# Optimization experiments

Hardware: AMD Instinct MI355X
Metric: run time of the kernel (lower is better)

Reference implementation:

```python
import jax, jax.numpy as jnp
import numpy as np

B, DIN, N = 8, 256, 2048  # batch, input_dim (orig node_num), attention nodes (orig seq_len)


def setup_inputs() -> dict:
    key = jax.random.key(0)
    k1, k2, k3, k4 = jax.random.split(key, 4)
    x = jax.random.normal(k1, (B, DIN, N), jnp.float32)
    adj = jax.random.randint(k2, (N, N), 0, 2).astype(jnp.int32)  # binary adjacency
    W = jax.random.normal(k3, (DIN, DIN), jnp.float32) * 0.05      # Linear(D, D, bias=False), stored (out, in)
    a = jax.random.normal(k4, (3 * DIN,), jnp.float32) * 0.05      # Linear(3D, 1, bias=False)
    return {"x": x, "adj": adj, "W": W, "a": a}


def reference(x, adj, W, a):
    # x: (B, D, N) -> permute to (B, N, D); attention is over the N axis
    xt = jnp.transpose(x, (0, 2, 1))
    h = xt @ W.T                                   # (B, N, D)
    sim = jnp.einsum('bid,bjd->bij', h, h)         # (B, N, N) pairwise dot products
    n = adj.shape[0]
    # neighbor mask: adj nonzero, diagonal forced off (mask[:, i] = 0 in the loop)
    m = (adj != 0) & (~jnp.eye(n, dtype=bool))
    # context: the torch loop's weighted_h is independent of its k axis, so
    # context[b, k, i, d] == C[b, i, d] = sum_j m[i,j] * sim[b,i,j] * h[b,j,d]
    C = jnp.einsum('bij,bjd->bid', jnp.where(m[None, :, :], sim, 0.0), h)  # (B, N, D)
    d = h.shape[-1]
    a1, a2, a3 = a[:d], a[d:2 * d], a[2 * d:]
    # a([h_i, h_j, C_j]) = a1.h_i + a2.h_j + a3.C_j  (concat never materialized)
    s_i = h @ a1                                   # (B, N)
    s_j = h @ a2 + C @ a3                          # (B, N)
    scores = jax.nn.leaky_relu(s_i[:, :, None] + s_j[:, None, :], negative_slope=0.2)
    scores = jnp.where(adj[None, :, :] == 0, jnp.float32(-9e15), scores)
    return jax.nn.softmax(scores, axis=-1)         # (B, N, N)
```

## Files before the change

### kernel.cpp

```cpp
#include <hip/hip_runtime.h>
#include <hip/hip_bf16.h>
#include <math.h>

#define Bq   8
#define DINq 256
#define Nq   2048

typedef __attribute__((ext_vector_type(8))) short bf16x8v;
typedef __attribute__((ext_vector_type(4))) float f32x4v;

__device__ __forceinline__ unsigned short f2bf(float f) {
  union { float f; unsigned u; } v; v.f = f;
  unsigned r = v.u + 0x7fffu + ((v.u >> 16) & 1u);
  return (unsigned short)(r >> 16);
}
__device__ __forceinline__ float bf2f(unsigned short h) {
  union { unsigned u; float f; } v; v.u = ((unsigned)h) << 16;
  return v.f;
}

__device__ __forceinline__ void gld_lds16(const void* g, void* l) {
  __builtin_amdgcn_global_load_lds(
      (const __attribute__((address_space(1))) unsigned int*)g,
      (__attribute__((address_space(3))) unsigned int*)l, 16, 0, 0);
}

__device__ __forceinline__ bf16x8v expand_mask(unsigned m8) {
  union { unsigned u[4]; bf16x8v v; } r;
  unsigned lo4 = ((m8 & 0xFu) * 0x204081u) & 0x01010101u;
  unsigned hi4 = (((m8 >> 4) & 0xFu) * 0x204081u) & 0x01010101u;
  r.u[0] = ((lo4 & 0xFFu) | ((lo4 & 0xFF00u) << 8)) * 0x3F80u;
  r.u[1] = (((lo4 >> 16) & 0xFFu) | ((lo4 >> 24) << 16)) * 0x3F80u;
  r.u[2] = ((hi4 & 0xFFu) | ((hi4 & 0xFF00u) << 8)) * 0x3F80u;
  r.u[3] = (((hi4 >> 16) & 0xFFu) | ((hi4 >> 24) << 16)) * 0x3F80u;
  return r.v;
}

__global__ void k_prep(const float* __restrict__ W, const float* __restrict__ a,
                       float* __restrict__ w123) {
  __shared__ float red[3][4][256];
  const int k = threadIdx.x & 255, dq = threadIdx.x >> 8;
  float s1 = 0.f, s2 = 0.f, s3 = 0.f;
  for (int d = dq * 64; d < dq * 64 + 64; ++d) {
    float w = W[d * DINq + k];
    s1 += w * a[d];
    s2 += w * a[DINq + d];
    s3 += w * a[2 * DINq + d];
  }
  red[0][dq][k] = s1; red[1][dq][k] = s2; red[2][dq][k] = s3;
  __syncthreads();
  if (threadIdx.x < 256) {
    w123[k]            = red[0][0][k] + red[0][1][k] + red[0][2][k] + red[0][3][k];
    w123[DINq + k]     = red[1][0][k] + red[1][1][k] + red[1][2][k] + red[1][3][k];
    w123[2 * DINq + k] = red[2][0][k] + red[2][1][k] + red[2][2][k] + red[2][3][k];
  }
}

__global__ void k_transposeW(const float* __restrict__ W, float* __restrict__ WT) {
  int d = blockIdx.x, k = threadIdx.x;
  WT[(size_t)k * DINq + d] = W[(size_t)d * DINq + k];
}

__global__ __launch_bounds__(256, 2) void k_hX(const float* __restrict__ x,
                     const float* __restrict__ WT, const float* __restrict__ w123,
                     unsigned short* __restrict__ Xhi, unsigned short* __restrict__ Xlo,
                     float* __restrict__ tA, float* __restrict__ siA,
                     float* __restrict__ sbA) {
  __shared__ float xs[64][32];
  __shared__ float ws[64][128];
  __shared__ float wls[3][256];
  __shared__ float Pd[3][16][32];
  __shared__ float Tt[32];
  const int tid = threadIdx.x;
  const int iq = tid & 15;
  const int dg = tid >> 4;
  const int i0 = blockIdx.x * 32;
  const int b = blockIdx.y;

  for (int n = tid; n < 768; n += 256) ((float*)wls)[n] = w123[n];

  float p1[2] = {0.f, 0.f}, p2[2] = {0.f, 0.f}, p3[2] = {0.f, 0.f};

#pragma unroll
  for (int dh = 0; dh < 2; ++dh) {
    float acc[2][8];
#pragma unroll
    for (int aa = 0; aa < 2; ++aa)
#pragma unroll
      for (int cc = 0; cc < 8; ++cc) acc[aa][cc] = 0.f;

    for (int kc = 0; kc < 4; ++kc) {
      __syncthreads();
#pragma unroll
      for (int n = 0; n < 8; ++n) {
        int idx = n * 256 + tid;
        int kk = idx >> 5, ii = idx & 31;
        xs[kk][ii] = x[((size_t)b * DINq + kc * 64 + kk) * Nq + i0 + ii];
      }
#pragma unroll
      for (int n = 0; n < 8; ++n) {
        int idx = n * 256 + tid;
        int kk = idx >> 5, c4 = (idx & 31) * 4;
        *(f32x4v*)&ws[kk][c4] =
            *(const f32x4v*)&WT[(size_t)(kc * 64 + kk) * DINq + dh * 128 + c4];
      }
      __syncthreads();
#pragma unroll 4
      for (int kk = 0; kk < 64; ++kk) {
        float xv0 = xs[kk][iq * 2], xv1 = xs[kk][iq * 2 + 1];
        f32x4v w0 = *(const f32x4v*)&ws[kk][dg * 8];
        f32x4v w1 = *(const f32x4v*)&ws[kk][dg * 8 + 4];
#pragma unroll
        for (int cc = 0; cc < 4; ++cc) {
          acc[0][cc]     += xv0 * w0[cc];
          acc[0][cc + 4] += xv0 * w1[cc];
          acc[1][cc]     += xv1 * w0[cc];
          acc[1][cc + 4] += xv1 * w1[cc];
        }
      }
      if (dh == 0) {
#pragma unroll
        for (int kap = 0; kap < 4; ++kap) {
          int kk = dg * 4 + kap;
          float xv0 = xs[kk][iq * 2], xv1 = xs[kk][iq * 2 + 1];
          float w3 = wls[2][kc * 64 + kk];
          float w1v = wls[0][kc * 64 + kk], w2v = wls[1][kc * 64 + kk];
          p3[0] += xv0 * w3;  p3[1] += xv1 * w3;
          p1[0] += xv0 * w1v; p1[1] += xv1 * w1v;
          p2[0] += xv0 * w2v; p2[1] += xv1 * w2v;
        }
      }
    }

    if (dh == 0) {
#pragma unroll
      for (int aa = 0; aa < 2; ++aa) {
        Pd[0][dg][iq * 2 + aa] = p1[aa];
        Pd[1][dg][iq * 2 + aa] = p2[aa];
        Pd[2][dg][iq * 2 + aa] = p3[aa];
      }
      __syncthreads();
      if (tid < 32) {
        float t = 0.f, s1 = 0.f, s2 = 0.f;
#pragma unroll
        for (int g = 0; g < 16; ++g) {
          s1 += Pd[0][g][tid]; s2 += Pd[1][g][tid]; t += Pd[2][g][tid];
        }
        Tt[tid] = t;
        tA[(size_t)b * Nq + i0 + tid] = t;
        siA[(size_t)b * Nq + i0 + tid] = s1;
        sbA[(size_t)b * Nq + i0 + tid] = s2;
      }
      __syncthreads();
    }

    const float tv0 = Tt[iq * 2], tv1 = Tt[iq * 2 + 1];
#pragma unroll
    for (int cc = 0; cc < 8; ++cc) {
      int d = dh * 128 + dg * 8 + cc;
      float X0 = tv0 * acc[0][cc];
      float X1 = tv1 * acc[1][cc];
      unsigned short h0 = f2bf(X0), h1 = f2bf(X1);
      unsigned short l0 = f2bf(X0 - bf2f(h0)), l1 = f2bf(X1 - bf2f(h1));
      size_t xoff = ((size_t)b * DINq + d) * Nq + i0 + iq * 2;
      *(ushort2*)&Xhi[xoff] = make_ushort2(h0, h1);
      *(ushort2*)&Xlo[xoff] = make_ushort2(l0, l1);
    }
  }
}

__global__ void k_mask(const int* __restrict__ adj, unsigned* __restrict__ bm) {
  int wg = blockIdx.x * 256 + threadIdx.x;
  int i = wg >> 6, w = wg & 63, j0 = w * 32;
  const int4* ap = (const int4*)&adj[(size_t)i * Nq + j0];
  unsigned bits = 0;
#pragma unroll
  for (int q = 0; q < 8; ++q) {
    int4 a = ap[q];
    if (a.x) bits |= 1u << (q * 4);
    if (a.y) bits |= 1u << (q * 4 + 1);
    if (a.z) bits |= 1u << (q * 4 + 2);
    if (a.w) bits |= 1u << (q * 4 + 3);
  }
  bm[wg] = bits;
}

__global__ __launch_bounds__(256, 2) void k_gemm(const unsigned* __restrict__ bm,
                                                 const unsigned short* __restrict__ Xhi,
                                                 const unsigned short* __restrict__ Xlo,
                                                 float* __restrict__ sjp) {
  __shared__ __align__(16) unsigned short Bs[3][2][128 * 32];
  __shared__ unsigned bmlds[256 * 16];
  const int tid = threadIdx.x;
  const int lane = tid & 63;
  const int wave = tid >> 6;
  const int wm = wave >> 1, wc = wave & 1;
  const int wg = blockIdx.x;
  const int xcd = wg & 7;
  const int sub = wg >> 3;
  const int ct = xcd * 2 + (sub & 1);
  const int mt = (sub >> 1) & 7;
  const int ks = sub >> 4;
  const int i0 = mt * 256, c0 = ct * 128, kbase = ks * 512;
  const int r15 = lane & 15, kg = lane >> 4;
  const int kb = 16 * (kg ^ ((r15 >> 1) & 3));

  {
    const int kw0 = kbase >> 5;
#pragma unroll
    for (int n = 0; n < 4; ++n) {
      int idx4 = n * 256 + tid;
      int r = idx4 >> 2, w4 = (idx4 & 3) * 4;
      uint4 v = *(const uint4*)&bm[(size_t)(i0 + r) * 64 + kw0 + w4];
      bmlds[r * 16 + ((w4 + 0) ^ (r & 15))] = v.x;
      bmlds[r * 16 + ((w4 + 1) ^ (r & 15))] = v.y;
      bmlds[r * 16 + ((w4 + 2) ^ (r & 15))] = v.z;
      bmlds[r * 16 + ((w4 + 3) ^ (r & 15))] = v.w;
    }
  }
  __syncthreads();

  f32x4v acc[8][4];
#pragma unroll
  for (int m = 0; m < 8; ++m)
#pragma unroll
    for (int n = 0; n < 4; ++n) acc[m][n] = (f32x4v)0.f;

  auto STAGE = [&](int buf, int t) {
    const int k0 = kbase + t * 32;
#pragma unroll
    for (int l = 0; l < 2; ++l) {
      const int pc = l * 256 + tid;
      const int row = pc >> 2, q = pc & 3;
      const int kc = 8 * (q ^ ((row >> 1) & 3));
      gld_lds16(&Xhi[(size_t)(c0 + row) * Nq + k0 + kc], &Bs[buf][0][pc * 8]);
      gld_lds16(&Xlo[(size_t)(c0 + row) * Nq + k0 + kc], &Bs[buf][1][pc * 8]);
    }
  };

  constexpr int NT = 16;
  STAGE(0, 0);
  STAGE(1, 1);
  int cb = 0, sb2 = 2;
  for (int t = 0; t < NT; ++t) {
    if (t + 1 < NT) {
      asm volatile("s_waitcnt vmcnt(4)" ::: "memory");
    } else {
      asm volatile("s_waitcnt vmcnt(0)" ::: "memory");
    }
    __builtin_amdgcn_sched_barrier(0);
    __builtin_amdgcn_s_barrier();
    __builtin_amdgcn_sched_barrier(0);
    if (t + 2 < NT) STAGE(sb2, t + 2);

    const char* Bh = (const char*)&Bs[cb][0][0];
    const char* Bl = (const char*)&Bs[cb][1][0];
    bf16x8v bfh[4], bfl[4];
#pragma unroll
    for (int n = 0; n < 4; ++n) {
      bfh[n] = *(const bf16x8v*)(Bh + (wc * 64 + n * 16 + r15) * 64 + kb);
      bfl[n] = *(const bf16x8v*)(Bl + (wc * 64 + n * 16 + r15) * 64 + kb);
    }
    const int jb = kbase + t * 32 + kg * 8;
#pragma unroll
    for (int m = 0; m < 8; ++m) {
      const int arow = wm * 128 + m * 16 + r15;
      unsigned wv = bmlds[arow * 16 + (t ^ (arow & 15))];
      unsigned m8 = (wv >> (kg * 8)) & 0xFFu;
      unsigned d = (unsigned)(i0 + arow - jb);
      if (d < 8u) m8 &= ~(1u << d);
      bf16x8v af = expand_mask(m8);
      __builtin_amdgcn_s_setprio(1);
#pragma unroll
      for (int n = 0; n < 4; ++n) {
        acc[m][n] = __builtin_amdgcn_mfma_f32_16x16x32_bf16(af, bfh[n], acc[m][n], 0, 0, 0);
        acc[m][n] = __builtin_amdgcn_mfma_f32_16x16x32_bf16(af, bfl[n], acc[m][n], 0, 0, 0);
      }
      __builtin_amdgcn_s_setprio(0);
    }
    cb = (cb == 2) ? 0 : cb + 1;
    sb2 = (sb2 == 2) ? 0 : sb2 + 1;
  }

  const int b = c0 >> 8;
  const int re = (lane >> 4) * 4, ce = lane & 15;
  float s[8][4];
#pragma unroll
  for (int m = 0; m < 8; ++m)
#pragma unroll
    for (int r = 0; r < 4; ++r) s[m][r] = 0.f;
#pragma unroll
  for (int n = 0; n < 4; ++n) {
    const size_t xrow = (size_t)(c0 + wc * 64 + n * 16 + ce) * Nq;
#pragma unroll
    for (int m = 0; m < 8; ++m) {
      const size_t ib = xrow + i0 + wm * 128 + m * 16 + re;
      ushort4 xh = *(const ushort4*)&Xhi[ib];
      ushort4 xl = *(const ushort4*)&Xlo[ib];
      s[m][0] += acc[m][n][0] * (bf2f(xh.x) + bf2f(xl.x));
      s[m][1] += acc[m][n][1] * (bf2f(xh.y) + bf2f(xl.y));
      s[m][2] += acc[m][n][2] * (bf2f(xh.z) + bf2f(xl.z));
      s[m][3] += acc[m][n][3] * (bf2f(xh.w) + bf2f(xl.w));
    }
  }
#pragma unroll
  for (int o = 1; o < 16; o <<= 1) {
#pragma unroll
    for (int m = 0; m < 8; ++m)
#pragma unroll
      for (int r = 0; r < 4; ++r) s[m][r] += __shfl_xor(s[m][r], o, 64);
  }
  if (ce == 0) {
    const int slice = (ct & 1) * 8 + ks * 2 + wc;
    float* sp = sjp + ((size_t)slice * Bq + b) * Nq;
#pragma unroll
    for (int m = 0; m < 8; ++m)
#pragma unroll
      for (int r = 0; r < 4; ++r)
        sp[i0 + wm * 128 + m * 16 + re + r] = s[m][r];
  }
}

__global__ void k_sjsum(const float* __restrict__ sbA, const float* __restrict__ tA,
                        const float* __restrict__ sjp, float* __restrict__ sjvA) {
  int idx = blockIdx.x * 256 + threadIdx.x;
  float s = 0.f;
#pragma unroll
  for (int sl = 0; sl < 16; ++sl) s += sjp[(size_t)sl * Bq * Nq + idx];
  sjvA[idx] = sbA[idx] + s / tA[idx];
}

__global__ void k_softmax(const unsigned* __restrict__ bm, const float* __restrict__ siA,
                          const float* __restrict__ sjvA, float* __restrict__ out) {
  const int b = blockIdx.y, i = blockIdx.x, tid = threadIdx.x;
  const float siv = siA[(size_t)b * Nq + i];
  const unsigned* brow = bm + (size_t)i * 64;
  const float* sjb = sjvA + (size_t)b * Nq;
  const int bit = tid & 31;
  float sc[8];
  float mx = -3.0e38f;
#pragma unroll
  for (int s = 0; s < 8; ++s) {
    int j = s * 256 + tid;
    float v = siv + sjb[j];
    v = v > 0.f ? v : 0.2f * v;
    unsigned wv = brow[j >> 5];
    v = ((wv >> bit) & 1u) ? v : -9.0e15f;
    sc[s] = v;
    mx = fmaxf(mx, v);
  }
#pragma unroll
  for (int o = 32; o >= 1; o >>= 1) mx = fmaxf(mx, __shfl_xor(mx, o, 64));
  __shared__ float redm[4], reds[4];
  const int wave = tid >> 6, lane = tid & 63;
  if (lane == 0) redm[wave] = mx;
  __syncthreads();
  mx = fmaxf(fmaxf(redm[0], redm[1]), fmaxf(redm[2], redm[3]));
  float sum = 0.f, ex[8];
#pragma unroll
  for (int s = 0; s < 8; ++s) { ex[s] = expf(sc[s] - mx); sum += ex[s]; }
#pragma unroll
  for (int o = 32; o >= 1; o >>= 1) sum += __shfl_xor(sum, o, 64);
  if (lane == 0) reds[wave] = sum;
  __syncthreads();
  sum = reds[0] + reds[1] + reds[2] + reds[3];
  float inv = 1.f / sum;
  float* orow = out + ((size_t)b * Nq + i) * Nq;
#pragma unroll
  for (int s = 0; s < 8; ++s) orow[s * 256 + tid] = ex[s] * inv;
}

extern "C" void kernel_launch(void* const* d_in, const int* in_sizes, int n_in,
                              void* d_out, int out_size, void* d_ws, size_t ws_size,
                              hipStream_t stream) {
  const float* x = (const float*)d_in[0];
  const int* adj = (const int*)d_in[1];
  const float* W = (const float*)d_in[2];
  const float* a = (const float*)d_in[3];
  float* out = (float*)d_out;

  char* ws = (char*)d_ws;
  size_t off = 0;
  auto alloc = [&](size_t bytes) -> void* {
    void* p = ws + off;
    off += (bytes + 255) & ~(size_t)255;
    return p;
  };
  float* w123 = (float*)alloc(3 * DINq * sizeof(float));
  float* WT = (float*)alloc((size_t)DINq * DINq * sizeof(float));
  float* tA = (float*)alloc((size_t)Bq * Nq * sizeof(float));
  float* siA = (float*)alloc((size_t)Bq * Nq * sizeof(float));
  float* sbA = (float*)alloc((size_t)Bq * Nq * sizeof(float));
  float* sjvA = (float*)alloc((size_t)Bq * Nq * sizeof(float));
  float* sjp = (float*)alloc((size_t)16 * Bq * Nq * sizeof(float));
  unsigned short* Xhi = (unsigned short*)alloc((size_t)Nq * Nq * 2);
  unsigned short* Xlo = (unsigned short*)alloc((size_t)Nq * Nq * 2);
  unsigned* bm = (unsigned*)alloc((size_t)Nq * 64 * sizeof(unsigned));

  k_prep<<<dim3(1), dim3(1024), 0, stream>>>(W, a, w123);
  k_transposeW<<<dim3(DINq), dim3(DINq), 0, stream>>>(W, WT);
  k_hX<<<dim3(Nq / 32, Bq), dim3(256), 0, stream>>>(x, WT, w123, Xhi, Xlo, tA, siA, sbA);
  k_mask<<<dim3(Nq * 64 / 256), dim3(256), 0, stream>>>(adj, bm);
  k_gemm<<<dim3(512), dim3(256), 0, stream>>>(bm, Xhi, Xlo, sjp);
  k_sjsum<<<dim3(Bq * Nq / 256), dim3(256), 0, stream>>>(sbA, tA, sjp, sjvA);
  k_softmax<<<dim3(Nq, Bq), dim3(256), 0, stream>>>(bm, siA, sjvA, out);
}
```

Before: 134.4 us.

## Retile k_hX to 64x256 output tiles with direct-to-LDS loads

```diff
diff --git a/kernel.cpp b/kernel.cpp
--- a/kernel.cpp
+++ b/kernel.cpp
@@ -61,111 +61,100 @@
   WT[(size_t)k * DINq + d] = W[(size_t)d * DINq + k];
 }
 
-__global__ __launch_bounds__(256, 2) void k_hX(const float* __restrict__ x,
+__global__ __launch_bounds__(256, 1) void k_hX(const float* __restrict__ x,
                      const float* __restrict__ WT, const float* __restrict__ w123,
                      unsigned short* __restrict__ Xhi, unsigned short* __restrict__ Xlo,
                      float* __restrict__ tA, float* __restrict__ siA,
                      float* __restrict__ sbA) {
-  __shared__ float xs[64][32];
-  __shared__ float ws[64][128];
-  __shared__ float wls[3][256];
-  __shared__ float Pd[3][16][32];
-  __shared__ float Tt[32];
+  __shared__ float xs[64][64];
+  __shared__ float ws[64][256];
+  __shared__ float Tt[64];
   const int tid = threadIdx.x;
-  const int iq = tid & 15;
-  const int dg = tid >> 4;
-  const int i0 = blockIdx.x * 32;
+  const int iq = tid & 7;
+  const int dg = tid >> 3;
+  const int i0 = blockIdx.x * 64;
   const int b = blockIdx.y;
-
-  for (int n = tid; n < 768; n += 256) ((float*)wls)[n] = w123[n];
-
-  float p1[2] = {0.f, 0.f}, p2[2] = {0.f, 0.f}, p3[2] = {0.f, 0.f};
-
-#pragma unroll
-  for (int dh = 0; dh < 2; ++dh) {
-    float acc[2][8];
-#pragma unroll
-    for (int aa = 0; aa < 2; ++aa)
-#pragma unroll
-      for (int cc = 0; cc < 8; ++cc) acc[aa][cc] = 0.f;
-
-    for (int kc = 0; kc < 4; ++kc) {
-      __syncthreads();
-#pragma unroll
-      for (int n = 0; n < 8; ++n) {
-        int idx = n * 256 + tid;
-        int kk = idx >> 5, ii = idx & 31;
-        xs[kk][ii] = x[((size_t)b * DINq + kc * 64 + kk) * Nq + i0 + ii];
+  const bool w0 = (tid < 64);
+
+  float acc[8][8];
+#pragma unroll
+  for (int e = 0; e < 8; ++e)
+#pragma unroll
+    for (int cc = 0; cc < 8; ++cc) acc[e][cc] = 0.f;
+  float p1 = 0.f, p2 = 0.f, p3 = 0.f;
+
+  for (int kc = 0; kc < 4; ++kc) {
+    __syncthreads();
+#pragma unroll
+    for (int l = 0; l < 4; ++l) {
+      int c = l * 256 + tid;
+      int r = c >> 4, ch = c & 15;
+      gld_lds16(&x[((size_t)b * DINq + kc * 64 + r) * Nq + i0 + ch * 4], &xs[r][ch * 4]);
+    }
+#pragma unroll
+    for (int l = 0; l < 16; ++l) {
+      int c = l * 256 + tid;
+      int r = c >> 6, ch = c & 63;
+      gld_lds16(&WT[(size_t)(kc * 64 + r) * DINq + ch * 4], &ws[r][ch * 4]);
+    }
+    asm volatile("s_waitcnt vmcnt(0)" ::: "memory");
+    __syncthreads();
+#pragma unroll 4
+    for (int kk = 0; kk < 64; ++kk) {
+      f32x4v xv0 = *(const f32x4v*)&xs[kk][iq * 8];
+      f32x4v xv1 = *(const f32x4v*)&xs[kk][iq * 8 + 4];
+      f32x4v wv0 = *(const f32x4v*)&ws[kk][dg * 8];
+      f32x4v wv1 = *(const f32x4v*)&ws[kk][dg * 8 + 4];
+#pragma unroll
+      for (int ii = 0; ii < 4; ++ii) {
+#pragma unroll
+        for (int cc = 0; cc < 4; ++cc) {
+          acc[ii][cc]         += xv0[ii] * wv0[cc];
+          acc[ii][cc + 4]     += xv0[ii] * wv1[cc];
+          acc[ii + 4][cc]     += xv1[ii] * wv0[cc];
+          acc[ii + 4][cc + 4] += xv1[ii] * wv1[cc];
+        }
       }
-#pragma unroll
-      for (int n = 0; n < 8; ++n) {
-        int idx = n * 256 + tid;
-        int kk = idx >> 5, c4 = (idx & 31) * 4;
-        *(f32x4v*)&ws[kk][c4] =
-            *(const f32x4v*)&WT[(size_t)(kc * 64 + kk) * DINq + dh * 128 + c4];
-      }
-      __syncthreads();
+    }
+    if (w0) {
 #pragma unroll 4
       for (int kk = 0; kk < 64; ++kk) {
-        float xv0 = xs[kk][iq * 2], xv1 = xs[kk][iq * 2 + 1];
-        f32x4v w0 = *(const f32x4v*)&ws[kk][dg * 8];
-        f32x4v w1 = *(const f32x4v*)&ws[kk][dg * 8 + 4];
-#pragma unroll
-        for (int cc = 0; cc < 4; ++cc) {
-          acc[0][cc]     += xv0 * w0[cc];
-          acc[0][cc + 4] += xv0 * w1[cc];
-          acc[1][cc]     += xv1 * w0[cc];
-          acc[1][cc + 4] += xv1 * w1[cc];
-        }
+        float xv = xs[kk][tid];
+        p1 += xv * w123[kc * 64 + kk];
+        p2 += xv * w123[DINq + kc * 64 + kk];
+        p3 += xv * w123[2 * DINq + kc * 64 + kk];
       }
-      if (dh == 0) {
-#pragma unroll
-        for (int kap = 0; kap < 4; ++kap) {
-          int kk = dg * 4 + kap;
-          float xv0 = xs[kk][iq * 2], xv1 = xs[kk][iq * 2 + 1];
-          float w3 = wls[2][kc * 64 + kk];
-          float w1v = wls[0][kc * 64 + kk], w2v = wls[1][kc * 64 + kk];
-          p3[0] += xv0 * w3;  p3[1] += xv1 * w3;
-          p1[0] += xv0 * w1v; p1[1] += xv1 * w1v;
-          p2[0] += xv0 * w2v; p2[1] += xv1 * w2v;
-        }
-      }
-    }
-
-    if (dh == 0) {
-#pragma unroll
-      for (int aa = 0; aa < 2; ++aa) {
-        Pd[0][dg][iq * 2 + aa] = p1[aa];
-        Pd[1][dg][iq * 2 + aa] = p2[aa];
-        Pd[2][dg][iq * 2 + aa] = p3[aa];
-      }
-      __syncthreads();
-      if (tid < 32) {
-        float t = 0.f, s1 = 0.f, s2 = 0.f;
-#pragma unroll
-        for (int g = 0; g < 16; ++g) {
-          s1 += Pd[0][g][tid]; s2 += Pd[1][g][tid]; t += Pd[2][g][tid];
-        }
-        Tt[tid] = t;
-        tA[(size_t)b * Nq + i0 + tid] = t;
-        siA[(size_t)b * Nq + i0 + tid] = s1;
-        sbA[(size_t)b * Nq + i0 + tid] = s2;
-      }
-      __syncthreads();
-    }
-
-    const float tv0 = Tt[iq * 2], tv1 = Tt[iq * 2 + 1];
-#pragma unroll
-    for (int cc = 0; cc < 8; ++cc) {
-      int d = dh * 128 + dg * 8 + cc;
-      float X0 = tv0 * acc[0][cc];
-      float X1 = tv1 * acc[1][cc];
-      unsigned short h0 = f2bf(X0), h1 = f2bf(X1);
-      unsigned short l0 = f2bf(X0 - bf2f(h0)), l1 = f2bf(X1 - bf2f(h1));
-      size_t xoff = ((size_t)b * DINq + d) * Nq + i0 + iq * 2;
-      *(ushort2*)&Xhi[xoff] = make_ushort2(h0, h1);
-      *(ushort2*)&Xlo[xoff] = make_ushort2(l0, l1);
-    }
+    }
+  }
+
+  if (w0) {
+    Tt[tid] = p3;
+    tA[(size_t)b * Nq + i0 + tid] = p3;
+    siA[(size_t)b * Nq + i0 + tid] = p1;
+    sbA[(size_t)b * Nq + i0 + tid] = p2;
+  }
+  __syncthreads();
+
+  float tv[8];
+#pragma unroll
+  for (int e = 0; e < 8; ++e) tv[e] = Tt[iq * 8 + e];
+
+#pragma unroll
+  for (int cc = 0; cc < 8; ++cc) {
+    const int d = dg * 8 + cc;
+    unsigned short hv[8], lv[8];
+#pragma unroll
+    for (int e = 0; e < 8; ++e) {
+      float Xv = tv[e] * acc[e][cc];
+      unsigned short hs = f2bf(Xv);
+      hv[e] = hs;
+      lv[e] = f2bf(Xv - bf2f(hs));
+    }
+    size_t off = ((size_t)b * DINq + d) * Nq + i0 + iq * 8;
+    *(ushort4*)&Xhi[off]     = make_ushort4(hv[0], hv[1], hv[2], hv[3]);
+    *(ushort4*)&Xhi[off + 4] = make_ushort4(hv[4], hv[5], hv[6], hv[7]);
+    *(ushort4*)&Xlo[off]     = make_ushort4(lv[0], lv[1], lv[2], lv[3]);
+    *(ushort4*)&Xlo[off + 4] = make_ushort4(lv[4], lv[5], lv[6], lv[7]);
   }
 }
 
@@ -399,7 +388,7 @@
 
   k_prep<<<dim3(1), dim3(1024), 0, stream>>>(W, a, w123);
   k_transposeW<<<dim3(DINq), dim3(DINq), 0, stream>>>(W, WT);
-  k_hX<<<dim3(Nq / 32, Bq), dim3(256), 0, stream>>>(x, WT, w123, Xhi, Xlo, tA, siA, sbA);
+  k_hX<<<dim3(Nq / 64, Bq), dim3(256), 0, stream>>>(x, WT, w123, Xhi, Xlo, tA, siA, sbA);
   k_mask<<<dim3(Nq * 64 / 256), dim3(256), 0, stream>>>(adj, bm);
   k_gemm<<<dim3(512), dim3(256), 0, stream>>>(bm, Xhi, Xlo, sjp);
   k_sjsum<<<dim3(Bq * Nq / 256), dim3(256), 0, stream>>>(sbA, tA, sjp, sjvA);
```

Result: no change. 136.7 us (+1.7%).

## Split GEMM K range in half and stage hi/lo bf16 tiles alternately

Applied to the files above, without the earlier changes.

```diff
diff --git a/kernel.cpp b/kernel.cpp
--- a/kernel.cpp
+++ b/kernel.cpp
@@ -185,12 +185,13 @@
   bm[wg] = bits;
 }
 
-__global__ __launch_bounds__(256, 2) void k_gemm(const unsigned* __restrict__ bm,
+__global__ __launch_bounds__(256, 4) void k_gemm(const unsigned* __restrict__ bm,
                                                  const unsigned short* __restrict__ Xhi,
                                                  const unsigned short* __restrict__ Xlo,
                                                  float* __restrict__ sjp) {
-  __shared__ __align__(16) unsigned short Bs[3][2][128 * 32];
-  __shared__ unsigned bmlds[256 * 16];
+  __shared__ __align__(16) unsigned short Bs[3][128 * 32];
+  __shared__ unsigned bmlds[256 * 8];
+  __shared__ float swb[8][128];
   const int tid = threadIdx.x;
   const int lane = tid & 63;
   const int wave = tid >> 6;
@@ -201,21 +202,21 @@
   const int ct = xcd * 2 + (sub & 1);
   const int mt = (sub >> 1) & 7;
   const int ks = sub >> 4;
-  const int i0 = mt * 256, c0 = ct * 128, kbase = ks * 512;
+  const int i0 = mt * 256, c0 = ct * 128, kbase = ks * 256;
   const int r15 = lane & 15, kg = lane >> 4;
   const int kb = 16 * (kg ^ ((r15 >> 1) & 3));
 
   {
     const int kw0 = kbase >> 5;
 #pragma unroll
-    for (int n = 0; n < 4; ++n) {
+    for (int n = 0; n < 2; ++n) {
       int idx4 = n * 256 + tid;
-      int r = idx4 >> 2, w4 = (idx4 & 3) * 4;
+      int r = idx4 >> 1, w4 = (idx4 & 1) * 4;
       uint4 v = *(const uint4*)&bm[(size_t)(i0 + r) * 64 + kw0 + w4];
-      bmlds[r * 16 + ((w4 + 0) ^ (r & 15))] = v.x;
-      bmlds[r * 16 + ((w4 + 1) ^ (r & 15))] = v.y;
-      bmlds[r * 16 + ((w4 + 2) ^ (r & 15))] = v.z;
-      bmlds[r * 16 + ((w4 + 3) ^ (r & 15))] = v.w;
+      bmlds[r * 8 + ((w4 + 0) ^ (r & 7))] = v.x;
+      bmlds[r * 8 + ((w4 + 1) ^ (r & 7))] = v.y;
+      bmlds[r * 8 + ((w4 + 2) ^ (r & 7))] = v.z;
+      bmlds[r * 8 + ((w4 + 3) ^ (r & 7))] = v.w;
     }
   }
   __syncthreads();
@@ -227,14 +228,14 @@
     for (int n = 0; n < 4; ++n) acc[m][n] = (f32x4v)0.f;
 
   auto STAGE = [&](int buf, int t) {
-    const int k0 = kbase + t * 32;
+    const unsigned short* __restrict__ src = (t & 1) ? Xlo : Xhi;
+    const int k0 = kbase + (t >> 1) * 32;
 #pragma unroll
     for (int l = 0; l < 2; ++l) {
       const int pc = l * 256 + tid;
       const int row = pc >> 2, q = pc & 3;
       const int kc = 8 * (q ^ ((row >> 1) & 3));
-      gld_lds16(&Xhi[(size_t)(c0 + row) * Nq + k0 + kc], &Bs[buf][0][pc * 8]);
-      gld_lds16(&Xlo[(size_t)(c0 + row) * Nq + k0 + kc], &Bs[buf][1][pc * 8]);
+      gld_lds16(&src[(size_t)(c0 + row) * Nq + k0 + kc], &Bs[buf][pc * 8]);
     }
   };
 
@@ -244,7 +245,7 @@
   int cb = 0, sb2 = 2;
   for (int t = 0; t < NT; ++t) {
     if (t + 1 < NT) {
-      asm volatile("s_waitcnt vmcnt(4)" ::: "memory");
+      asm volatile("s_waitcnt vmcnt(2)" ::: "memory");
     } else {
       asm volatile("s_waitcnt vmcnt(0)" ::: "memory");
     }
@@ -253,29 +254,25 @@
     __builtin_amdgcn_sched_barrier(0);
     if (t + 2 < NT) STAGE(sb2, t + 2);
 
-    const char* Bh = (const char*)&Bs[cb][0][0];
-    const char* Bl = (const char*)&Bs[cb][1][0];
-    bf16x8v bfh[4], bfl[4];
-#pragma unroll
-    for (int n = 0; n < 4; ++n) {
-      bfh[n] = *(const bf16x8v*)(Bh + (wc * 64 + n * 16 + r15) * 64 + kb);
-      bfl[n] = *(const bf16x8v*)(Bl + (wc * 64 + n * 16 + r15) * 64 + kb);
-    }
-    const int jb = kbase + t * 32 + kg * 8;
+    const char* Bb = (const char*)&Bs[cb][0];
+    bf16x8v bf[4];
+#pragma unroll
+    for (int n = 0; n < 4; ++n)
+      bf[n] = *(const bf16x8v*)(Bb + (wc * 64 + n * 16 + r15) * 64 + kb);
+    const int kch = t >> 1;
+    const int jb = kbase + kch * 32 + kg * 8;
 #pragma unroll
     for (int m = 0; m < 8; ++m) {
       const int arow = wm * 128 + m * 16 + r15;
-      unsigned wv = bmlds[arow * 16 + (t ^ (arow & 15))];
+      unsigned wv = bmlds[arow * 8 + (kch ^ (arow & 7))];
       unsigned m8 = (wv >> (kg * 8)) & 0xFFu;
       unsigned d = (unsigned)(i0 + arow - jb);
       if (d < 8u) m8 &= ~(1u << d);
       bf16x8v af = expand_mask(m8);
       __builtin_amdgcn_s_setprio(1);
 #pragma unroll
-      for (int n = 0; n < 4; ++n) {
-        acc[m][n] = __builtin_amdgcn_mfma_f32_16x16x32_bf16(af, bfh[n], acc[m][n], 0, 0, 0);
-        acc[m][n] = __builtin_amdgcn_mfma_f32_16x16x32_bf16(af, bfl[n], acc[m][n], 0, 0, 0);
-      }
+      for (int n = 0; n < 4; ++n)
+        acc[m][n] = __builtin_amdgcn_mfma_f32_16x16x32_bf16(af, bf[n], acc[m][n], 0, 0, 0);
       __builtin_amdgcn_s_setprio(0);
     }
     cb = (cb == 2) ? 0 : cb + 1;
@@ -311,13 +308,18 @@
       for (int r = 0; r < 4; ++r) s[m][r] += __shfl_xor(s[m][r], o, 64);
   }
   if (ce == 0) {
-    const int slice = (ct & 1) * 8 + ks * 2 + wc;
-    float* sp = sjp + ((size_t)slice * Bq + b) * Nq;
 #pragma unroll
     for (int m = 0; m < 8; ++m)
 #pragma unroll
       for (int r = 0; r < 4; ++r)
-        sp[i0 + wm * 128 + m * 16 + re + r] = s[m][r];
+        swb[wave][m * 16 + re + r] = s[m][r];
+  }
+  __builtin_amdgcn_s_barrier();
+  {
+    const int slice = (ct & 1) * 16 + ks * 2 + wc;
+    float* sp = sjp + ((size_t)slice * Bq + b) * Nq + i0 + wm * 128;
+    sp[lane] = swb[wave][lane];
+    sp[64 + lane] = swb[wave][64 + lane];
   }
 }
 
@@ -326,7 +328,7 @@
   int idx = blockIdx.x * 256 + threadIdx.x;
   float s = 0.f;
 #pragma unroll
-  for (int sl = 0; sl < 16; ++sl) s += sjp[(size_t)sl * Bq * Nq + idx];
+  for (int sl = 0; sl < 32; ++sl) s += sjp[(size_t)sl * Bq * Nq + idx];
   sjvA[idx] = sbA[idx] + s / tA[idx];
 }
 
@@ -392,7 +394,7 @@
   float* siA = (float*)alloc((size_t)Bq * Nq * sizeof(float));
   float* sbA = (float*)alloc((size_t)Bq * Nq * sizeof(float));
   float* sjvA = (float*)alloc((size_t)Bq * Nq * sizeof(float));
-  float* sjp = (float*)alloc((size_t)16 * Bq * Nq * sizeof(float));
+  float* sjp = (float*)alloc((size_t)32 * Bq * Nq * sizeof(float));
   unsigned short* Xhi = (unsigned short*)alloc((size_t)Nq * Nq * 2);
   unsigned short* Xlo = (unsigned short*)alloc((size_t)Nq * Nq * 2);
   unsigned* bm = (unsigned*)alloc((size_t)Nq * 64 * sizeof(unsigned));
@@ -401,7 +403,7 @@
   k_transposeW<<<dim3(DINq), dim3(DINq), 0, stream>>>(W, WT);
   k_hX<<<dim3(Nq / 32, Bq), dim3(256), 0, stream>>>(x, WT, w123, Xhi, Xlo, tA, siA, sbA);
   k_mask<<<dim3(Nq * 64 / 256), dim3(256), 0, stream>>>(adj, bm);
-  k_gemm<<<dim3(512), dim3(256), 0, stream>>>(bm, Xhi, Xlo, sjp);
+  k_gemm<<<dim3(1024), dim3(256), 0, stream>>>(bm, Xhi, Xlo, sjp);
   k_sjsum<<<dim3(Bq * Nq / 256), dim3(256), 0, stream>>>(sbA, tA, sjp, sjvA);
   k_softmax<<<dim3(Nq, Bq), dim3(256), 0, stream>>>(bm, siA, sjvA, out);
 }
```

Result: slower. 361.8 us (+169.1%).
